# Optimization experiments

Measured on AMD Instinct MI355X. Metric: run time of the kernel, lower is better.

The kernel has to match this reference:

```python
import jax, jax.numpy as jnp
import numpy as np

NUM_HEADS = 16
DEPTH = 0


def rotate_half(x):
    x1, x2 = jnp.split(x, 2, axis=-1)
    return jnp.concatenate((-x2, x1), axis=-1)


def rotary_tables(seq_len, rot_dim, dtype):
    # RotaryEmbedding(dim=rot_dim): inv_freq over even indices of rot_dim
    inv_freq = 1.0 / (10000.0 ** (jnp.arange(0, rot_dim, 2, dtype=jnp.float32) / rot_dim))
    freqs = jnp.arange(seq_len, dtype=jnp.float32)[:, None] * inv_freq[None, :]  # [N, rot_dim/2]
    emb = jnp.concatenate((freqs, freqs), axis=-1)  # [N, rot_dim]
    return emb.astype(dtype), jnp.cos(emb).astype(dtype), jnp.sin(emb).astype(dtype)


def setup_inputs() -> dict:
    key = jax.random.key(0)
    ks = jax.random.split(key, 7)
    B, N, C = 1, 2048, 1024
    hd = C // NUM_HEADS
    std_qkv = (1.0 / C) ** 0.5
    std_proj = (1.0 / (2 * C)) ** 0.5
    return {
        "x": jax.random.normal(ks[0], (B, N, C), dtype=jnp.float32),
        "W_qkv": jax.random.normal(ks[1], (6 * C, C), dtype=jnp.float32) * std_qkv,
        "W_proj": jax.random.normal(ks[2], (C, 2 * C), dtype=jnp.float32) * std_proj,
        "lambda_q1": jax.random.normal(ks[3], (hd,), dtype=jnp.float32) * 0.1,
        "lambda_q2": jax.random.normal(ks[4], (hd,), dtype=jnp.float32) * 0.1,
        "lambda_k1": jax.random.normal(ks[5], (hd,), dtype=jnp.float32) * 0.1,
        "lambda_k2": jax.random.normal(ks[6], (hd,), dtype=jnp.float32) * 0.1,
    }


def reference(x, W_qkv, W_proj, lambda_q1, lambda_q2, lambda_k1, lambda_k2):
    B, N, C = x.shape
    H = NUM_HEADS
    hd = C // H
    scale = hd ** -0.5
    lambda_init = 0.8 - 0.6 * np.exp(-0.3 * DEPTH)

    qkv = jnp.einsum('bnc,dc->bnd', x, W_qkv)               # [B,N,6C]
    qkv = qkv.reshape(B, N, 6, H, hd).transpose(2, 0, 3, 1, 4)  # [6,B,H,N,hd]
    q = jnp.concatenate((qkv[0], qkv[1]), axis=-1)          # [B,H,N,2hd]
    k = jnp.concatenate((qkv[2], qkv[3]), axis=-1)
    v = jnp.concatenate((qkv[4], qkv[5]), axis=-1)

    _, cos, sin = rotary_tables(N, 2 * hd, x.dtype)          # [N,2hd]
    q = q * cos + rotate_half(q) * sin
    k = k * cos + rotate_half(k) * sin

    q1, q2 = jnp.split(q, 2, axis=-1)                        # [B,H,N,hd] each
    k1, k2 = jnp.split(k, 2, axis=-1)

    attn1 = jnp.einsum('bhid,bhjd->bhij', q1, k1) * scale
    attn2 = jnp.einsum('bhid,bhjd->bhij', q2, k2) * scale

    lam1 = jnp.exp(jnp.sum(lambda_q1 * lambda_k1))
    lam2 = jnp.exp(jnp.sum(lambda_q2 * lambda_k2))
    lam = (lam1 - lam2 + lambda_init).astype(x.dtype)

    probs = jax.nn.softmax(attn1, axis=-1) - lam * jax.nn.softmax(attn2, axis=-1)
    out = jnp.einsum('bhij,bhjd->bhid', probs, v)            # [B,H,N,2hd]
    out = out.transpose(0, 2, 1, 3).reshape(B, N, 2 * C)
    out = jnp.einsum('bnd,cd->bnc', out, W_proj)             # [B,N,C]
    return out
```

## Files before the change

kernel.cpp:

```cpp
#include <hip/hip_runtime.h>

using bf16_t = __bf16;
typedef __bf16 bf16x8 __attribute__((ext_vector_type(8)));
typedef float floatx4 __attribute__((ext_vector_type(4)));

#define MFMA_BF16(a, b, c) __builtin_amdgcn_mfma_f32_16x16x32_bf16((a), (b), (c), 0, 0, 0)

__device__ __forceinline__ void async_ld16(bf16_t* lds_dst, const bf16_t* g_src) {
    __builtin_amdgcn_global_load_lds(
        (const __attribute__((address_space(1))) void*)g_src,
        (__attribute__((address_space(3))) void*)lds_dst, 16, 0, 0);
}

__global__ __launch_bounds__(256) void cast_bf16(const float* __restrict__ src,
                                                 bf16_t* __restrict__ dst, int n8) {
    int i = blockIdx.x * 256 + threadIdx.x;
    if (i < n8) {
        const floatx4 a = *(const floatx4*)(src + (size_t)i * 8);
        const floatx4 b = *(const floatx4*)(src + (size_t)i * 8 + 4);
        bf16x8 r;
        r[0] = (bf16_t)a[0]; r[1] = (bf16_t)a[1]; r[2] = (bf16_t)a[2]; r[3] = (bf16_t)a[3];
        r[4] = (bf16_t)b[0]; r[5] = (bf16_t)b[1]; r[6] = (bf16_t)b[2]; r[7] = (bf16_t)b[3];
        *(bf16x8*)(dst + (size_t)i * 8) = r;
    }
}

__global__ void lam_kernel(const float* lq1, const float* lq2,
                           const float* lk1, const float* lk2, float* lamp) {
    int l = threadIdx.x;
    float p1 = lq1[l] * lk1[l];
    float p2 = lq2[l] * lk2[l];
    #pragma unroll
    for (int d = 1; d < 64; d <<= 1) {
        p1 += __shfl_xor(p1, d);
        p2 += __shfl_xor(p2, d);
    }
    if (l == 0) *lamp = expf(p1) - expf(p2) + 0.2f;
}

template <int BM, int BN, bool QKV_EPI, typename TC>
__global__ __launch_bounds__(256) void gemm_bt(const bf16_t* __restrict__ A,
                                               const bf16_t* __restrict__ B,
                                               TC* __restrict__ C,
                                               bf16_t* __restrict__ Qb,
                                               bf16_t* __restrict__ Kb,
                                               bf16_t* __restrict__ Vt,
                                               int M, int N, int K) {
    constexpr int BK = 32;
    __shared__ __align__(16) bf16_t As[BM * BK];
    __shared__ __align__(16) bf16_t Bs[BN * BK];
    const int t = threadIdx.x;
    const int lane = t & 63, wave = t >> 6;
    const int q4 = lane >> 4, m16 = lane & 15;
    const int mblk = blockIdx.y * BM, nblk = blockIdx.x * BN;
    const int wr = wave >> 1, wc = wave & 1;
    constexpr int WM = BM / 2, WN = BN / 2;
    constexpr int NI = WM / 16, NJ = WN / 16;
    constexpr int AR = BM * BK / 2048;
    constexpr int BR = BN * BK / 2048;

    floatx4 acc[NI][NJ] = {};

    for (int k0 = 0; k0 < K; k0 += BK) {
        __syncthreads();
        #pragma unroll
        for (int rr = 0; rr < AR; ++rr) {
            int f = rr * 256 + t;
            async_ld16(&As[f * 8], &A[(size_t)(mblk + (f >> 2)) * K + k0 + (f & 3) * 8]);
        }
        #pragma unroll
        for (int rr = 0; rr < BR; ++rr) {
            int f = rr * 256 + t;
            async_ld16(&Bs[f * 8], &B[(size_t)(nblk + (f >> 2)) * K + k0 + (f & 3) * 8]);
        }
        __syncthreads();

        bf16x8 a[NI], b[NJ];
        #pragma unroll
        for (int i = 0; i < NI; ++i)
            a[i] = *(const bf16x8*)&As[(wr * WM + i * 16 + m16) * 32 + q4 * 8];
        #pragma unroll
        for (int j = 0; j < NJ; ++j)
            b[j] = *(const bf16x8*)&Bs[(wc * WN + j * 16 + m16) * 32 + q4 * 8];
        #pragma unroll
        for (int i = 0; i < NI; ++i)
            #pragma unroll
            for (int j = 0; j < NJ; ++j)
                acc[i][j] = MFMA_BF16(a[i], b[j], acc[i][j]);
    }

    #pragma unroll
    for (int i = 0; i < NI; ++i)
        #pragma unroll
        for (int j = 0; j < NJ; ++j) {
            int n = nblk + wc * WN + j * 16 + m16;
            #pragma unroll
            for (int r = 0; r < 4; ++r) {
                int m = mblk + wr * WM + i * 16 + q4 * 4 + r;
                if constexpr (QKV_EPI) {
                    bf16_t val = (bf16_t)acc[i][j][r];
                    int comp = n >> 10, h = (n >> 6) & 15, e = n & 63;
                    if (comp < 2)
                        Qb[(size_t)((comp * 16 + h) * 2048 + m) * 64 + e] = val;
                    else if (comp < 4)
                        Kb[(size_t)(((comp - 2) * 16 + h) * 2048 + m) * 64 + e] = val;
                    else
                        Vt[(size_t)(h * 128 + (comp - 4) * 64 + e) * 2048 + m] = val;
                } else {
                    C[(size_t)m * N + n] = (TC)acc[i][j][r];
                }
            }
        }
}

__global__ __launch_bounds__(256) void rotary_inplace(bf16_t* __restrict__ Qb,
                                                      bf16_t* __restrict__ Kb) {
    int t = blockIdx.x * 256 + threadIdx.x;
    int e = t & 63, h = (t >> 6) & 15, n = t >> 10;
    float invf = exp2f(-(float)e * (13.287712379549449f / 64.0f));
    float ang = (float)n * invf;
    float s, c;
    sincosf(ang, &s, &c);
    int off = (h * 2048 + n) * 64 + e;
    float q1 = (float)Qb[off], q2 = (float)Qb[off + 2097152];
    Qb[off]           = (bf16_t)(q1 * c - q2 * s);
    Qb[off + 2097152] = (bf16_t)(q2 * c + q1 * s);
    float k1 = (float)Kb[off], k2 = (float)Kb[off + 2097152];
    Kb[off]           = (bf16_t)(k1 * c - k2 * s);
    Kb[off + 2097152] = (bf16_t)(k2 * c + k1 * s);
}

__global__ __launch_bounds__(512, 4) void flash_diff(const bf16_t* __restrict__ Qb,
                                                     const bf16_t* __restrict__ Kb,
                                                     const bf16_t* __restrict__ Vt,
                                                     const float* __restrict__ lamp,
                                                     bf16_t* __restrict__ Ao) {
    constexpr int N = 2048, BN = 64;
    __shared__ __align__(16) bf16_t smem[24576];
    bf16_t* Kf = smem;
    bf16_t* Vf = smem + 8192;
    bf16_t* Pf = smem + 16384;
    const int t = threadIdx.x, lane = t & 63, w = t >> 6;
    const int comp = w >> 2, w4 = w & 3;
    const int q4 = lane >> 4, m16 = lane & 15;
    const int Lb = blockIdx.x;
    const int virt = (Lb & 7) * 64 + (Lb >> 3);
    const int h = virt >> 5, qt = virt & 31;
    const float lam = *lamp;
    const float cexp = 0.125f * 1.4426950408889634f;

    bf16x8 qf[2];
    const int qrow = qt * 64 + w4 * 16 + m16;
    #pragma unroll
    for (int kc = 0; kc < 2; ++kc)
        qf[kc] = *(const bf16x8*)&Qb[(size_t)((comp * 16 + h) * 2048 + qrow) * 64 + kc * 32 + q4 * 8];

    bf16x8 ones;
    #pragma unroll
    for (int j = 0; j < 8; ++j) ones[j] = (bf16_t)1.0f;

    floatx4 O[8] = {};
    floatx4 sm = {};

    for (int k0 = 0; k0 < N; k0 += BN) {
        __syncthreads();
        #pragma unroll
        for (int rr = 0; rr < 4; ++rr) {
            int idx = w * 4 + rr;
            if (idx < 16) {
                int i = idx >> 3, s = (idx >> 1) & 3, half = idx & 1;
                async_ld16(&Kf[idx * 512],
                           &Kb[(size_t)((i * 16 + h) * 2048 + k0 + 16 * s + m16) * 64 + half * 32 + q4 * 8]);
            } else {
                int v = idx - 16, tt = v >> 1, half = v & 1;
                async_ld16(&Vf[v * 512],
                           &Vt[(size_t)(h * 128 + tt * 16 + m16) * 2048 + k0 + half * 32 + q4 * 8]);
            }
        }
        __syncthreads();

        bf16_t* pw = &Pf[w * 1024];
        #pragma unroll
        for (int s = 0; s < 4; ++s) {
            floatx4 sacc = {};
            const bf16x8 kf0 = *(const bf16x8*)&Kf[((comp * 4 + s) * 2 + 0) * 512 + lane * 8];
            const bf16x8 kf1 = *(const bf16x8*)&Kf[((comp * 4 + s) * 2 + 1) * 512 + lane * 8];
            sacc = MFMA_BF16(qf[0], kf0, sacc);
            sacc = MFMA_BF16(qf[1], kf1, sacc);
            const int half = s >> 1, quad = (2 * s + (m16 >> 3)) & 3, jj = m16 & 7;
            #pragma unroll
            for (int r = 0; r < 4; ++r) {
                int u = quad * 16 + q4 * 4 + r;
                pw[half * 512 + (u ^ quad) * 8 + jj] = (bf16_t)exp2f(sacc[r] * cexp);
            }
        }

        bf16x8 pf[2];
        const int ur = lane ^ q4;
        pf[0] = *(const bf16x8*)&pw[0 * 512 + ur * 8];
        pf[1] = *(const bf16x8*)&pw[1 * 512 + ur * 8];
        sm = MFMA_BF16(pf[0], ones, sm);
        sm = MFMA_BF16(pf[1], ones, sm);
        #pragma unroll
        for (int tt = 0; tt < 8; ++tt) {
            const bf16x8 vf0 = *(const bf16x8*)&Vf[(tt * 2 + 0) * 512 + lane * 8];
            const bf16x8 vf1 = *(const bf16x8*)&Vf[(tt * 2 + 1) * 512 + lane * 8];
            O[tt] = MFMA_BF16(pf[0], vf0, O[tt]);
            O[tt] = MFMA_BF16(pf[1], vf1, O[tt]);
        }
    }

    float inv[4];
    #pragma unroll
    for (int r = 0; r < 4; ++r) inv[r] = 1.0f / sm[r];

    float* Ff = (float*)smem;
    __syncthreads();
    if (comp == 1) {
        #pragma unroll
        for (int tt = 0; tt < 8; ++tt) {
            floatx4 val;
            #pragma unroll
            for (int r = 0; r < 4; ++r) val[r] = lam * O[tt][r] * inv[r];
            *(floatx4*)&Ff[((w4 * 128 + tt * 16 + m16) << 4) + q4 * 4] = val;
        }
    }
    __syncthreads();
    if (comp == 0) {
        const int orow = qt * 64 + w4 * 16 + q4 * 4;
        #pragma unroll
        for (int tt = 0; tt < 8; ++tt) {
            const floatx4 v1 = *(const floatx4*)&Ff[((w4 * 128 + tt * 16 + m16) << 4) + q4 * 4];
            #pragma unroll
            for (int r = 0; r < 4; ++r) {
                float val = O[tt][r] * inv[r] - v1[r];
                Ao[(size_t)(orow + r) * 2048 + h * 128 + tt * 16 + m16] = (bf16_t)val;
            }
        }
    }
}

extern "C" void kernel_launch(void* const* d_in, const int* in_sizes, int n_in,
                              void* d_out, int out_size, void* d_ws, size_t ws_size,
                              hipStream_t stream) {
    const float* x     = (const float*)d_in[0];
    const float* Wqkv  = (const float*)d_in[1];
    const float* Wproj = (const float*)d_in[2];
    const float* lq1   = (const float*)d_in[3];
    const float* lq2   = (const float*)d_in[4];
    const float* lk1   = (const float*)d_in[5];
    const float* lk2   = (const float*)d_in[6];
    float* out = (float*)d_out;

    char* ws = (char*)d_ws;
    bf16_t* xb     = (bf16_t*)(ws);
    bf16_t* Ao     = (bf16_t*)(ws);
    bf16_t* Wqkvb  = (bf16_t*)(ws + 4194304);
    bf16_t* Wprojb = (bf16_t*)(ws + 16777216);
    bf16_t* Qb     = (bf16_t*)(ws + 20971520);
    bf16_t* Kb     = (bf16_t*)(ws + 29360128);
    bf16_t* Vt     = (bf16_t*)(ws + 37748736);
    float*  lamp   = (float*)(ws + 46137344);

    lam_kernel<<<1, 64, 0, stream>>>(lq1, lq2, lk1, lk2, lamp);
    cast_bf16<<<1024, 256, 0, stream>>>(x, xb, 2048 * 1024 / 8);
    cast_bf16<<<3072, 256, 0, stream>>>(Wqkv, Wqkvb, 6144 * 1024 / 8);
    cast_bf16<<<1024, 256, 0, stream>>>(Wproj, Wprojb, 1024 * 2048 / 8);
    gemm_bt<128, 128, true, float><<<dim3(48, 16), 256, 0, stream>>>(
        xb, Wqkvb, (float*)nullptr, Qb, Kb, Vt, 2048, 6144, 1024);
    rotary_inplace<<<(2048 * 16 * 64) / 256, 256, 0, stream>>>(Qb, Kb);
    flash_diff<<<512, 512, 0, stream>>>(Qb, Kb, Vt, lamp, Ao);
    gemm_bt<128, 64, false, float><<<dim3(16, 16), 256, 0, stream>>>(
        Ao, Wprojb, out, (bf16_t*)nullptr, (bf16_t*)nullptr, (bf16_t*)nullptr,
        2048, 1024, 2048);
}
```

Baseline: 265.9 us.

## Double-buffer K/V tiles in flash_diff, add wave priority hints, vectorize Vt stores

The attention kernel now prefetches the next K/V tile into a second LDS buffer while the current tile is being computed. This removes one barrier per iteration and hides global-to-LDS load latency. s_setprio hints raise wave priority around the MFMA sections. The QKV GEMM epilogue writes the transposed V output as 4-wide bf16 vector stores instead of scalar stores. The trade-off is that LDS per block grows from 48KB to 80KB, which may reduce how many blocks fit on each CU.

```diff
diff --git a/kernel.cpp b/kernel.cpp
--- a/kernel.cpp
+++ b/kernel.cpp
@@ -1,6 +1,7 @@
 #include <hip/hip_runtime.h>
 
 using bf16_t = __bf16;
+typedef __bf16 bf16x4 __attribute__((ext_vector_type(4)));
 typedef __bf16 bf16x8 __attribute__((ext_vector_type(8)));
 typedef float floatx4 __attribute__((ext_vector_type(4)));
 
@@ -94,21 +95,29 @@
         #pragma unroll
         for (int j = 0; j < NJ; ++j) {
             int n = nblk + wc * WN + j * 16 + m16;
-            #pragma unroll
-            for (int r = 0; r < 4; ++r) {
-                int m = mblk + wr * WM + i * 16 + q4 * 4 + r;
-                if constexpr (QKV_EPI) {
-                    bf16_t val = (bf16_t)acc[i][j][r];
-                    int comp = n >> 10, h = (n >> 6) & 15, e = n & 63;
-                    if (comp < 2)
-                        Qb[(size_t)((comp * 16 + h) * 2048 + m) * 64 + e] = val;
-                    else if (comp < 4)
-                        Kb[(size_t)(((comp - 2) * 16 + h) * 2048 + m) * 64 + e] = val;
-                    else
-                        Vt[(size_t)(h * 128 + (comp - 4) * 64 + e) * 2048 + m] = val;
+            int mbase = mblk + wr * WM + i * 16 + q4 * 4;
+            if constexpr (QKV_EPI) {
+                int comp = n >> 10, h = (n >> 6) & 15, e = n & 63;
+                if (comp < 2) {
+                    #pragma unroll
+                    for (int r = 0; r < 4; ++r)
+                        Qb[(size_t)((comp * 16 + h) * 2048 + mbase + r) * 64 + e] =
+                            (bf16_t)acc[i][j][r];
+                } else if (comp < 4) {
+                    #pragma unroll
+                    for (int r = 0; r < 4; ++r)
+                        Kb[(size_t)(((comp - 2) * 16 + h) * 2048 + mbase + r) * 64 + e] =
+                            (bf16_t)acc[i][j][r];
                 } else {
-                    C[(size_t)m * N + n] = (TC)acc[i][j][r];
+                    bf16x4 pv;
+                    #pragma unroll
+                    for (int r = 0; r < 4; ++r) pv[r] = (bf16_t)acc[i][j][r];
+                    *(bf16x4*)&Vt[(size_t)(h * 128 + (comp - 4) * 64 + e) * 2048 + mbase] = pv;
                 }
+            } else {
+                #pragma unroll
+                for (int r = 0; r < 4; ++r)
+                    C[(size_t)(mbase + r) * N + n] = (TC)acc[i][j][r];
             }
         }
 }
@@ -135,11 +144,9 @@
                                                      const bf16_t* __restrict__ Vt,
                                                      const float* __restrict__ lamp,
                                                      bf16_t* __restrict__ Ao) {
-    constexpr int N = 2048, BN = 64;
-    __shared__ __align__(16) bf16_t smem[24576];
-    bf16_t* Kf = smem;
-    bf16_t* Vf = smem + 8192;
-    bf16_t* Pf = smem + 16384;
+    constexpr int N = 2048, BN = 64, NT = N / BN;
+    __shared__ __align__(16) bf16_t smem[40960];
+    bf16_t* Pf = smem + 32768;
     const int t = threadIdx.x, lane = t & 63, w = t >> 6;
     const int comp = w >> 2, w4 = w & 3;
     const int q4 = lane >> 4, m16 = lane & 15;
@@ -162,24 +169,36 @@
     floatx4 O[8] = {};
     floatx4 sm = {};
 
-    for (int k0 = 0; k0 < N; k0 += BN) {
-        __syncthreads();
+    auto stage = [&](bf16_t* Kd, bf16_t* Vd, int k0) {
         #pragma unroll
         for (int rr = 0; rr < 4; ++rr) {
             int idx = w * 4 + rr;
             if (idx < 16) {
                 int i = idx >> 3, s = (idx >> 1) & 3, half = idx & 1;
-                async_ld16(&Kf[idx * 512],
+                async_ld16(&Kd[idx * 512],
                            &Kb[(size_t)((i * 16 + h) * 2048 + k0 + 16 * s + m16) * 64 + half * 32 + q4 * 8]);
             } else {
                 int v = idx - 16, tt = v >> 1, half = v & 1;
-                async_ld16(&Vf[v * 512],
+                async_ld16(&Vd[v * 512],
                            &Vt[(size_t)(h * 128 + tt * 16 + m16) * 2048 + k0 + half * 32 + q4 * 8]);
             }
         }
+    };
+
+    stage(smem, smem + 8192, 0);
+
+    for (int it = 0; it < NT; ++it) {
+        const int cur = it & 1;
+        bf16_t* Kf = smem + cur * 16384;
+        bf16_t* Vf = Kf + 8192;
         __syncthreads();
+        if (it + 1 < NT) {
+            bf16_t* Kn = smem + (cur ^ 1) * 16384;
+            stage(Kn, Kn + 8192, (it + 1) * BN);
+        }
 
         bf16_t* pw = &Pf[w * 1024];
+        __builtin_amdgcn_s_setprio(1);
         #pragma unroll
         for (int s = 0; s < 4; ++s) {
             floatx4 sacc = {};
@@ -187,12 +206,14 @@
             const bf16x8 kf1 = *(const bf16x8*)&Kf[((comp * 4 + s) * 2 + 1) * 512 + lane * 8];
             sacc = MFMA_BF16(qf[0], kf0, sacc);
             sacc = MFMA_BF16(qf[1], kf1, sacc);
+            __builtin_amdgcn_s_setprio(0);
             const int half = s >> 1, quad = (2 * s + (m16 >> 3)) & 3, jj = m16 & 7;
             #pragma unroll
             for (int r = 0; r < 4; ++r) {
                 int u = quad * 16 + q4 * 4 + r;
                 pw[half * 512 + (u ^ quad) * 8 + jj] = (bf16_t)exp2f(sacc[r] * cexp);
             }
+            __builtin_amdgcn_s_setprio(1);
         }
 
         bf16x8 pf[2];
@@ -208,6 +229,7 @@
             O[tt] = MFMA_BF16(pf[0], vf0, O[tt]);
             O[tt] = MFMA_BF16(pf[1], vf1, O[tt]);
         }
+        __builtin_amdgcn_s_setprio(0);
     }
 
     float inv[4];
```

After: 253.3 us. -4.7%, faster.
